# Optimization experiments

Measured on AMD Instinct MI355X. Metric: run time of the kernel, lower is better.

## Reference

```python
import jax, jax.numpy as jnp
import numpy as np


def setup_inputs() -> dict:
    key = jax.random.key(0)
    kf, kx1, ky1, kw, kh = jax.random.split(key, 5)
    B, H, W, C, R = 4, 64, 64, 256, 128
    feature_map = jax.random.normal(kf, (B, H, W, C), dtype=jnp.float32)
    # valid boxes [x1,y1,x2,y2] with side lengths in [8,32] (>= 7x7 grid -> no empty bins)
    x1 = jax.random.uniform(kx1, (B, R), minval=0.0, maxval=W - 33.0)
    y1 = jax.random.uniform(ky1, (B, R), minval=0.0, maxval=H - 33.0)
    bw = jax.random.uniform(kw, (B, R), minval=8.0, maxval=32.0)
    bh = jax.random.uniform(kh, (B, R), minval=8.0, maxval=32.0)
    rois = jnp.stack([x1, y1, x1 + bw, y1 + bh], axis=-1)
    return {"feature_map": feature_map, "rois": rois, "pooling_h": 7, "pooling_w": 7}


def _bin_bounds(start, end, n):
    # start/end: int32 [B] absolute coords; returns (lo, hi) int32 [B, n] per-bin bounds.
    # Mirrors TF: float steps truncated to int32 (floor for nonneg); last bin ends at roi size.
    size = (end - start).astype(jnp.float32)            # [B]
    step = size / n
    k = jnp.arange(n, dtype=jnp.float32)                # [n]
    lo_rel = (k[None, :] * step[:, None]).astype(jnp.int32)
    hi_rel = jnp.where(jnp.arange(n)[None, :] + 1 < n,
                       ((k[None, :] + 1.0) * step[:, None]).astype(jnp.int32),
                       (end - start)[:, None])
    return start[:, None] + lo_rel, start[:, None] + hi_rel


def _roi_pool(feature_map, rois, ph, pw):
    B, H, W, C = feature_map.shape
    neg = jnp.array(-jnp.inf, feature_map.dtype)
    hidx = jnp.arange(H)
    widx = jnp.arange(W)

    def per_roi(carry, roi):  # roi: [B, 4] = [x1, y1, x2, y2]
        ws = jnp.maximum(jnp.round(roi[:, 0]).astype(jnp.int32), 0)
        hs = jnp.maximum(jnp.round(roi[:, 1]).astype(jnp.int32), 0)
        we = jnp.minimum(jnp.round(roi[:, 2]).astype(jnp.int32), W)
        he = jnp.minimum(jnp.round(roi[:, 3]).astype(jnp.int32), H)
        hlo, hhi = _bin_bounds(hs, he, ph)   # [B, ph]
        wlo, whi = _bin_bounds(ws, we, pw)   # [B, pw]
        mh = (hidx[None, None, :] >= hlo[:, :, None]) & (hidx[None, None, :] < hhi[:, :, None])  # [B,ph,H]
        mw = (widx[None, None, :] >= wlo[:, :, None]) & (widx[None, None, :] < whi[:, :, None])  # [B,pw,W]
        # masked max over w per w-bin, then over h per h-bin (bins partition the ROI)
        colmax = jnp.where(mw[:, :, None, :, None], feature_map[:, None], neg).max(axis=3)  # [B,pw,H,C]
        pooled = jnp.where(mh[:, :, None, :, None], colmax[:, None], neg).max(axis=3)       # [B,ph,pw,C]
        # TF code enumerates bins j-outer/i-inner but reshapes to (ph,pw): replicate that quirk.
        out = jnp.swapaxes(pooled, 1, 2).reshape(B, ph, pw, C)
        return carry, out

    _, outs = jax.lax.scan(per_roi, None, jnp.swapaxes(rois, 0, 1))  # [R,B,ph,pw,C]
    return jnp.swapaxes(outs, 0, 1)  # [B,R,ph,pw,C]


def reference(feature_map, rois, pooling_h, pooling_w):
    return _roi_pool(feature_map, rois, pooling_h, pooling_w)
```

## Files before the change

### kernel.cpp

```cpp
#include <hip/hip_runtime.h>
#include <math.h>

#define B 4
#define H 64
#define W 64
#define C 256
#define R 128
#define PH 7
#define PW 7

#define CELLS_TOTAL (B * R * PH * PW)
#define BLOCKS_TOTAL (CELLS_TOTAL / 4)
#define BLOCKS_PER_HALF 784

typedef float f32x4 __attribute__((ext_vector_type(4)));

__global__ __launch_bounds__(256) void roi_pool_kernel(
    const float* __restrict__ fm,
    const float* __restrict__ rois,
    float* __restrict__ out)
{
    const int wave = threadIdx.x >> 6;
    const int lane = threadIdx.x & 63;

    const int xcd  = blockIdx.x & 7;
    const int slot = blockIdx.x >> 3;
    const int b    = xcd >> 1;
    const int half = xcd & 1;
    const int cell_in_b = (half * BLOCKS_PER_HALF + slot) * 4 + wave;

    const int q = cell_in_b % PW;
    int t = cell_in_b / PW;
    const int p = t % PH;
    const int r = t / PH;

    const int ridx = __builtin_amdgcn_readfirstlane(b * R + r);
    const float* roi = rois + (size_t)ridx * 4;
    const float x1 = roi[0], y1 = roi[1], x2 = roi[2], y2 = roi[3];

    int ws = max((int)rintf(x1), 0);
    int hs = max((int)rintf(y1), 0);
    int we = min((int)rintf(x2), W);
    int he = min((int)rintf(y2), H);

    const float hstep = (float)(he - hs) / 7.0f;
    const float wstep = (float)(we - ws) / 7.0f;
    const int hlo = hs + (int)((float)q * hstep);
    const int hhi = (q < PH - 1) ? (hs + (int)((float)(q + 1) * hstep)) : he;
    const int wlo = ws + (int)((float)p * wstep);
    const int whi = (p < PW - 1) ? (ws + (int)((float)(p + 1) * wstep)) : we;

    const int nw = whi - wlo;
    const int nh = hhi - hlo;
    const int n  = nh * nw;

    const float* gp = fm + ((size_t)(b * H + hlo) * W + wlo) * C + lane * 4;
    int gw = 0;
    const size_t rstep = (size_t)(W - nw + 1) * C;

    f32x4 acc = { -INFINITY, -INFINITY, -INFINITY, -INFINITY };

#define LOADV(dst) (dst) = *(const f32x4*)gp
#define ADV() { if (++gw == nw) { gw = 0; gp += rstep; } else { gp += (size_t)C; } }
#define FM(vv) { acc.x = fmaxf(acc.x, (vv).x); acc.y = fmaxf(acc.y, (vv).y); \
                 acc.z = fmaxf(acc.z, (vv).z); acc.w = fmaxf(acc.w, (vv).w); }

    if (n >= 4) {
        f32x4 v0, v1, v2, v3;
        LOADV(v0); ADV(); LOADV(v1); ADV(); LOADV(v2); ADV(); LOADV(v3); ADV();
        int k = n - 4;
        while (k >= 4) {
            FM(v0); LOADV(v0); ADV();
            FM(v1); LOADV(v1); ADV();
            FM(v2); LOADV(v2); ADV();
            FM(v3); LOADV(v3); ADV();
            k -= 4;
        }
        if (k > 0) { FM(v0); LOADV(v0); ADV(); }
        if (k > 1) { FM(v1); LOADV(v1); ADV(); }
        if (k > 2) { FM(v2); LOADV(v2); ADV(); }
        FM(v0); FM(v1); FM(v2); FM(v3);
    } else {
        for (int i = 0; i < n; ++i) {
            f32x4 v; LOADV(v); ADV(); FM(v);
        }
    }

    const int cell = ((b * R + r) * PH + p) * PW + q;
    float* op = out + (size_t)cell * C + lane * 4;
    __builtin_nontemporal_store(acc, (f32x4*)op);
}

extern "C" void kernel_launch(void* const* d_in, const int* in_sizes, int n_in,
                              void* d_out, int out_size, void* d_ws, size_t ws_size,
                              hipStream_t stream) {
    const float* fm   = (const float*)d_in[0];
    const float* rois = (const float*)d_in[1];
    float* out = (float*)d_out;

    roi_pool_kernel<<<BLOCKS_TOTAL, 256, 0, stream>>>(fm, rois, out);
}
```

Baseline: 15.33 us.

## Process a full column strip of bins per wave, streaming bins sequentially

Each wave now handles one (roi, p) strip covering all seven q bins instead of a single bin. It walks the entire ROI height sequentially, emits a store whenever a bin's element count runs out, and resets the accumulator. This cuts the number of blocks by a factor of seven and amortises ROI and bin-bound setup across bins. The cost is less parallelism, with 3584 waves where there were 25088, and longer serial per-wave load chains, which may lower the ability to hide memory latency.

```diff
diff --git a/kernel.cpp b/kernel.cpp
--- a/kernel.cpp
+++ b/kernel.cpp
@@ -9,9 +9,10 @@
 #define PH 7
 #define PW 7
 
-#define CELLS_TOTAL (B * R * PH * PW)
-#define BLOCKS_TOTAL (CELLS_TOTAL / 4)
-#define BLOCKS_PER_HALF 784
+#define STRIPS_PER_BATCH (R * PH)
+#define BLOCKS_PER_BATCH (STRIPS_PER_BATCH / 4)
+#define BLOCKS_PER_XCD   (BLOCKS_PER_BATCH / 2)
+#define BLOCKS_TOTAL     (BLOCKS_PER_BATCH * B)
 
 typedef float f32x4 __attribute__((ext_vector_type(4)));
 
@@ -27,68 +28,79 @@
     const int slot = blockIdx.x >> 3;
     const int b    = xcd >> 1;
     const int half = xcd & 1;
-    const int cell_in_b = (half * BLOCKS_PER_HALF + slot) * 4 + wave;
-
-    const int q = cell_in_b % PW;
-    int t = cell_in_b / PW;
-    const int p = t % PH;
-    const int r = t / PH;
+    const int strip = (half * BLOCKS_PER_XCD + slot) * 4 + wave;
+    const int p = strip % PH;
+    const int r = strip / PH;
 
     const int ridx = __builtin_amdgcn_readfirstlane(b * R + r);
     const float* roi = rois + (size_t)ridx * 4;
     const float x1 = roi[0], y1 = roi[1], x2 = roi[2], y2 = roi[3];
 
-    int ws = max((int)rintf(x1), 0);
-    int hs = max((int)rintf(y1), 0);
-    int we = min((int)rintf(x2), W);
-    int he = min((int)rintf(y2), H);
+    const int ws_ = max((int)rintf(x1), 0);
+    const int hs_ = max((int)rintf(y1), 0);
+    const int we_ = min((int)rintf(x2), W);
+    const int he_ = min((int)rintf(y2), H);
 
-    const float hstep = (float)(he - hs) / 7.0f;
-    const float wstep = (float)(we - ws) / 7.0f;
-    const int hlo = hs + (int)((float)q * hstep);
-    const int hhi = (q < PH - 1) ? (hs + (int)((float)(q + 1) * hstep)) : he;
-    const int wlo = ws + (int)((float)p * wstep);
-    const int whi = (p < PW - 1) ? (ws + (int)((float)(p + 1) * wstep)) : we;
+    const float hstep = (float)(he_ - hs_) / 7.0f;
+    const float wstep = (float)(we_ - ws_) / 7.0f;
+    const int wlo = ws_ + (int)((float)p * wstep);
+    const int whi = (p < PW - 1) ? (ws_ + (int)((float)(p + 1) * wstep)) : we_;
+    const int nw  = whi - wlo;
 
-    const int nw = whi - wlo;
-    const int nh = hhi - hlo;
-    const int n  = nh * nw;
-
-    const float* gp = fm + ((size_t)(b * H + hlo) * W + wlo) * C + lane * 4;
+    const float* gp = fm + ((size_t)(b * H + hs_) * W + wlo) * C + lane * 4;
     int gw = 0;
     const size_t rstep = (size_t)(W - nw + 1) * C;
+
+    float* obase = out + ((size_t)((b * R + r) * PH + p) * PW) * C + lane * 4;
+
+    const int total = (he_ - hs_) * nw;
+
+    int q = 0;
+    int hprev = hs_;
+    int hnext = hs_ + (int)(hstep);
+    int binleft = (hnext - hprev) * nw;
 
     f32x4 acc = { -INFINITY, -INFINITY, -INFINITY, -INFINITY };
 
 #define LOADV(dst) (dst) = *(const f32x4*)gp
 #define ADV() { if (++gw == nw) { gw = 0; gp += rstep; } else { gp += (size_t)C; } }
-#define FM(vv) { acc.x = fmaxf(acc.x, (vv).x); acc.y = fmaxf(acc.y, (vv).y); \
-                 acc.z = fmaxf(acc.z, (vv).z); acc.w = fmaxf(acc.w, (vv).w); }
+#define CONSUME(vv) { \
+    acc.x = fmaxf(acc.x, (vv).x); acc.y = fmaxf(acc.y, (vv).y); \
+    acc.z = fmaxf(acc.z, (vv).z); acc.w = fmaxf(acc.w, (vv).w); \
+    if (--binleft == 0) { \
+        __builtin_nontemporal_store(acc, (f32x4*)(obase + (size_t)q * C)); \
+        acc.x = -INFINITY; acc.y = -INFINITY; acc.z = -INFINITY; acc.w = -INFINITY; \
+        ++q; \
+        if (q < 7) { \
+            hprev = hnext; \
+            hnext = (q < 6) ? (hs_ + (int)((float)(q + 1) * hstep)) : he_; \
+            binleft = (hnext - hprev) * nw; \
+        } \
+    } }
 
-    if (n >= 4) {
+    if (total >= 4) {
         f32x4 v0, v1, v2, v3;
         LOADV(v0); ADV(); LOADV(v1); ADV(); LOADV(v2); ADV(); LOADV(v3); ADV();
-        int k = n - 4;
+        int k = total - 4;
         while (k >= 4) {
-            FM(v0); LOADV(v0); ADV();
-            FM(v1); LOADV(v1); ADV();
-            FM(v2); LOADV(v2); ADV();
-            FM(v3); LOADV(v3); ADV();
+            CONSUME(v0); LOADV(v0); ADV();
+            CONSUME(v1); LOADV(v1); ADV();
+            CONSUME(v2); LOADV(v2); ADV();
+            CONSUME(v3); LOADV(v3); ADV();
             k -= 4;
         }
-        if (k > 0) { FM(v0); LOADV(v0); ADV(); }
-        if (k > 1) { FM(v1); LOADV(v1); ADV(); }
-        if (k > 2) { FM(v2); LOADV(v2); ADV(); }
-        FM(v0); FM(v1); FM(v2); FM(v3);
+        if (k > 0) { CONSUME(v0); LOADV(v0); ADV(); }
+        if (k > 1) { CONSUME(v1); LOADV(v1); ADV(); }
+        if (k > 2) { CONSUME(v2); LOADV(v2); ADV(); }
+        if (k == 0)      { CONSUME(v0); CONSUME(v1); CONSUME(v2); CONSUME(v3); }
+        else if (k == 1) { CONSUME(v1); CONSUME(v2); CONSUME(v3); CONSUME(v0); }
+        else if (k == 2) { CONSUME(v2); CONSUME(v3); CONSUME(v0); CONSUME(v1); }
+        else             { CONSUME(v3); CONSUME(v0); CONSUME(v1); CONSUME(v2); }
     } else {
-        for (int i = 0; i < n; ++i) {
-            f32x4 v; LOADV(v); ADV(); FM(v);
+        for (int i = 0; i < total; ++i) {
+            f32x4 v; LOADV(v); ADV(); CONSUME(v);
         }
     }
-
-    const int cell = ((b * R + r) * PH + p) * PW + q;
-    float* op = out + (size_t)cell * C + lane * 4;
-    __builtin_nontemporal_store(acc, (f32x4*)op);
 }
 
 extern "C" void kernel_launch(void* const* d_in, const int* in_sizes, int n_in,
```

Measured after the change: 26.24 us. +71.1%, slower.
